# Performance work log

Hardware: AMD Instinct MI355X
Metric: run time of the kernel (lower is better)

Reference implementation:

```python
import jax, jax.numpy as jnp
import numpy as np


def setup_inputs() -> dict:
    key = jax.random.key(0)
    k1, k2 = jax.random.split(key)
    x = jax.random.normal(k1, (4, 4096, 128), dtype=jnp.float32)
    kernel = jax.random.normal(k2, (3, 128, 64), dtype=jnp.float32)
    return {"x": x, "kernel": kernel}


def reference(x, kernel):
    # QKV projections: x [B,N,Din] @ kernel[i] [Din,Dout] -> [B,N,Dout]
    WQ = jnp.einsum('bnd,de->bne', x, kernel[0])
    WK = jnp.einsum('bnd,de->bne', x, kernel[1])
    WV = jnp.einsum('bnd,de->bne', x, kernel[2])
    d_out = WV.shape[-1]
    # scaled dot-product scores [B,N,N]
    scores = jnp.einsum('bqe,bke->bqk', WQ, WK) / jnp.sqrt(jnp.float32(d_out))
    attn = jax.nn.softmax(scores, axis=-1)
    return jnp.einsum('bqk,bke->bqe', attn, WV)
```

## Files before the change

kernel.cpp:

```cpp
#include <hip/hip_runtime.h>


typedef __attribute__((ext_vector_type(8))) short bf16x8;
typedef __attribute__((ext_vector_type(16))) float f32x16;
typedef __attribute__((ext_vector_type(4))) unsigned u32x4;
typedef unsigned short us;

__device__ __forceinline__ us f2bf(float f) {
  unsigned u = __builtin_bit_cast(unsigned, f);
  u += 0x7FFFu + ((u >> 16) & 1u);
  return (us)(u >> 16);
}
__device__ __forceinline__ float bf2f(us h) {
  unsigned u = ((unsigned)h) << 16;
  return __builtin_bit_cast(float, u);
}
__device__ __forceinline__ f32x16 mfma(bf16x8 a, bf16x8 b, f32x16 c) {
  return __builtin_amdgcn_mfma_f32_32x32x16_bf16(a, b, c, 0, 0, 0);
}
__device__ __forceinline__ unsigned pk2t(float a, float b) {
  return __builtin_amdgcn_perm(__builtin_bit_cast(unsigned, b),
                               __builtin_bit_cast(unsigned, a), 0x07060302u);
}
__device__ __forceinline__ void dma16(const us* g, us* l) {
  __builtin_amdgcn_global_load_lds(
      (const __attribute__((address_space(1))) unsigned*)g,
      (__attribute__((address_space(3))) unsigned*)l, 16, 0, 0);
}
#define EXP2(x) __builtin_amdgcn_exp2f(x)

#define NSEG 16
#define ITERS 4

__global__ __launch_bounds__(256, 1) void wprep_kernel(
    const float* __restrict__ w, us* __restrict__ Wbh, us* __restrict__ Wbl)
{
  const int i = blockIdx.x * 256 + threadIdx.x;
  if (i >= 24576) return;
  const int p = i >> 13, d = (i & 8191) >> 6, e = i & 63;
  float v = w[i];
  if (p == 0) v *= 0.18033688011112042f;
  const us hi = f2bf(v);
  const us lo = f2bf(v - bf2f(hi));
  const int g = (p * 64 + e) >> 5, ks = d >> 4, hh = (d >> 3) & 1, j = d & 7;
  const int o = ((g * 8 + ks) * 2 + hh) * 256 + (e & 31) * 8 + j;
  Wbh[o] = hi;
  Wbl[o] = lo;
}

__global__ __launch_bounds__(384, 1) void qkv_kernel(
    const float* __restrict__ x,
    const us* __restrict__ Wbh, const us* __restrict__ Wbl,
    us* __restrict__ Qhi, us* __restrict__ Qlo,
    us* __restrict__ Kbh, us* __restrict__ Kbl, us* __restrict__ Vb)
{
  __shared__ unsigned ttile[32 * 193];
  const int t = threadIdx.x;
  const int rb = blockIdx.x;
  const int wid = t >> 6, lane = t & 63;
  const int l31 = lane & 31, h = lane >> 5;
  const int rbase = rb * 32;
  const float* xrow = x + (size_t)(rbase + l31) * 128;

  f32x16 acc = {};
  #pragma unroll
  for (int ks = 0; ks < 8; ++ks) {
    const int d0 = ks * 16 + h * 8;
    const float4 xa = *(const float4*)(xrow + d0);
    const float4 xb = *(const float4*)(xrow + d0 + 4);
    const float xv[8] = {xa.x, xa.y, xa.z, xa.w, xb.x, xb.y, xb.z, xb.w};
    bf16x8 ah, al;
    #pragma unroll
    for (int j = 0; j < 8; ++j) {
      us hi = f2bf(xv[j]);
      ah[j] = (short)hi;
      al[j] = (short)f2bf(xv[j] - bf2f(hi));
    }
    const int wo = ((wid * 8 + ks) * 2 + h) * 256 + l31 * 8;
    bf16x8 bh = *(const bf16x8*)(Wbh + wo);
    bf16x8 bl = *(const bf16x8*)(Wbl + wo);
    acc = mfma(ah, bh, acc);
    acc = mfma(al, bh, acc);
    acc = mfma(ah, bl, acc);
  }

  #pragma unroll
  for (int r = 0; r < 16; ++r) {
    const int rl = (r & 3) + 8 * (r >> 2) + 4 * h;
    float v = acc[r];
    us hi = f2bf(v);
    us lo = f2bf(v - bf2f(hi));
    ttile[rl * 193 + wid * 32 + l31] = (unsigned)hi | ((unsigned)lo << 16);
  }
  __syncthreads();

  if (t < 64) {
    const int row = t >> 1, cb = (t & 1) * 32;
    const int grow = rbase + row;
    unsigned hw[16], lw[16];
    #pragma unroll
    for (int j = 0; j < 16; ++j) {
      unsigned a = ttile[row * 193 + cb + 2 * j];
      unsigned bv = ttile[row * 193 + cb + 2 * j + 1];
      hw[j] = (a & 0xffffu) | (bv << 16);
      lw[j] = (a >> 16) | (bv & 0xffff0000u);
    }
    #pragma unroll
    for (int j = 0; j < 4; ++j) {
      uint4 hv = {hw[4 * j], hw[4 * j + 1], hw[4 * j + 2], hw[4 * j + 3]};
      uint4 lv = {lw[4 * j], lw[4 * j + 1], lw[4 * j + 2], lw[4 * j + 3]};
      *(uint4*)(Qhi + (size_t)grow * 64 + cb + 8 * j) = hv;
      *(uint4*)(Qlo + (size_t)grow * 64 + cb + 8 * j) = lv;
    }
  } else if (t < 192) {
    const int bb = rbase >> 12;
    const int kt = (rbase & 4095) >> 6;
    const int m = (rbase >> 5) & 1;
    const size_t kbb = (size_t)bb * 262144 + (size_t)kt * 4096 + m * 256;
    #pragma unroll
    for (int i2 = 0; i2 < 2; ++i2) {
      const int c = (t - 64) + 128 * i2;
      const int r = c & 31, hh = (c >> 5) & 1, ks = c >> 6;
      unsigned hw[4], lw[4];
      #pragma unroll
      for (int j = 0; j < 4; ++j) {
        unsigned a = ttile[r * 193 + 64 + 16 * ks + 8 * hh + 2 * j];
        unsigned bv = ttile[r * 193 + 64 + 16 * ks + 8 * hh + 2 * j + 1];
        hw[j] = (a & 0xffffu) | (bv << 16);
        lw[j] = (a >> 16) | (bv & 0xffff0000u);
      }
      const size_t off = kbb + (size_t)(ks * 4 + 2 * hh) * 256 + r * 8;
      uint4 hv = {hw[0], hw[1], hw[2], hw[3]};
      uint4 lv = {lw[0], lw[1], lw[2], lw[3]};
      *(uint4*)(Kbh + off) = hv;
      *(uint4*)(Kbl + off) = lv;
    }
  } else if (t < 320) {
    const int bb = rbase >> 12;
    const int nb = rbase & 4095;
    #pragma unroll
    for (int i2 = 0; i2 < 2; ++i2) {
      const int c = (t - 192) + 128 * i2;
      const int e = c >> 2, nc = c & 3;
      unsigned p[4];
      #pragma unroll
      for (int j = 0; j < 4; ++j) {
        unsigned a = ttile[(nc * 8 + 2 * j) * 193 + 128 + e];
        unsigned bv = ttile[(nc * 8 + 2 * j + 1) * 193 + 128 + e];
        p[j] = (a & 0xffffu) | (bv << 16);
      }
      uint4 pv = {p[0], p[1], p[2], p[3]};
      const int n0 = nb + nc * 8;
      const int kt = n0 >> 6, sub = n0 & 63;
      const int ks = sub >> 4, hh = (sub >> 3) & 1;
      const int dt = e >> 5, lv = e & 31;
      *(uint4*)(Vb + (size_t)bb * 262144 +
                ((((kt * 4 + ks) * 2 + hh) * 2 + dt) * 256 + lv * 8)) = pv;
    }
  }
}

__global__ __launch_bounds__(256, 3) void attn_kernel(
    const us* __restrict__ Qhi, const us* __restrict__ Qlo,
    const us* __restrict__ Kbh, const us* __restrict__ Kbl,
    const us* __restrict__ Vb,
    us* __restrict__ Opart, float* __restrict__ Mpart,
    float* __restrict__ Lpart)
{
  __shared__ us stage[2][12288];
  __shared__ float alds[4][32];

  const int bx = blockIdx.x;
  const int xc = bx & 7, b = xc >> 1;
  const int idx = ((bx >> 3) << 1) | (xc & 1);
  const int seg = idx & (NSEG - 1), qg = idx >> 4;
  const int t = threadIdx.x;
  const int wid = t >> 6, lane = t & 63;
  const int l31 = lane & 31, h = lane >> 5;
  const int q0 = qg * 128 + wid * 32;
  const int u = (b * 4096 + q0) >> 5;
  const size_t pb = (size_t)u * NSEG + seg;

  bf16x8 qh[4], ql[4];
  {
    const size_t rg = (size_t)(b * 4096 + q0 + l31) * 64;
    #pragma unroll
    for (int ks = 0; ks < 4; ++ks) {
      qh[ks] = *(const bf16x8*)(Qhi + rg + ks * 16 + h * 8);
      ql[ks] = *(const bf16x8*)(Qlo + rg + ks * 16 + h * 8);
    }
  }
  const size_t kbase = (size_t)b * 262144;

  {
    const size_t kb0 = kbase + (size_t)(seg * ITERS) * 4096;
    #pragma unroll
    for (int i = 0; i < 6; ++i) {
      const int c = wid * 6 + i;
      const us* src = (c < 8)  ? Kbh + kb0 + c * 512
                    : (c < 16) ? Kbl + kb0 + (c - 8) * 512
                               : Vb  + kb0 + (c - 16) * 512;
      dma16(src + lane * 8, &stage[0][c * 512]);
    }
  }
  __syncthreads();

  f32x16 o[2] = {};
  float mrun = -__builtin_inff();
  float lrun = 0.f;

  for (int it = 0; it < ITERS; ++it) {
    const int cur = it & 1;
    const us* sb = &stage[cur][0];

    if (it + 1 < ITERS) {
      const size_t kbn = kbase + (size_t)(seg * ITERS + it + 1) * 4096;
      #pragma unroll
      for (int i = 0; i < 6; ++i) {
        const int c = wid * 6 + i;
        const us* src = (c < 8)  ? Kbh + kbn + c * 512
                      : (c < 16) ? Kbl + kbn + (c - 8) * 512
                                 : Vb  + kbn + (c - 16) * 512;
        dma16(src + lane * 8, &stage[cur ^ 1][c * 512]);
      }
    }

    f32x16 s[2] = {};
    __builtin_amdgcn_s_setprio(1);
    #pragma unroll
    for (int ks = 0; ks < 4; ++ks) {
      #pragma unroll
      for (int m = 0; m < 2; ++m) {
        const int ko = (ks * 4 + 2 * h + m) * 256 + l31 * 8;
        const bf16x8 ah = *(const bf16x8*)(sb + ko);
        const bf16x8 al = *(const bf16x8*)(sb + 4096 + ko);
        s[m] = mfma(ah, qh[ks], s[m]);
        s[m] = mfma(al, qh[ks], s[m]);
        s[m] = mfma(ah, ql[ks], s[m]);
      }
    }
    __builtin_amdgcn_s_setprio(0);

    float va = fmaxf(s[0][0], s[1][0]);
    float vb = fmaxf(s[0][1], s[1][1]);
    #pragma unroll
    for (int r = 2; r < 16; r += 2) {
      va = fmaxf(va, fmaxf(s[0][r], s[1][r]));
      vb = fmaxf(vb, fmaxf(s[0][r + 1], s[1][r + 1]));
    }
    float vm = fmaxf(va, vb);
    vm = fmaxf(vm, __shfl_xor(vm, 32));

    if (!__all(vm <= mrun - 24.f)) {
      const float mnew = (vm > mrun + 0.5f) ? vm : mrun;
      const float alpha = EXP2(mrun - mnew);
      float sm0 = 0.f, sm1 = 0.f;
      unsigned pp[2][8];
      #pragma unroll
      for (int m = 0; m < 2; ++m) {
        #pragma unroll
        for (int p = 0; p < 8; ++p) {
          const float p0 = EXP2(s[m][2 * p] - mnew);
          const float p1 = EXP2(s[m][2 * p + 1] - mnew);
          sm0 += p0;
          sm1 += p1;
          pp[m][p] = pk2t(p0, p1);
        }
      }
      float sum = sm0 + sm1;
      sum += __shfl_xor(sum, 32);
      lrun = lrun * alpha + sum;
      mrun = mnew;

      if (__any(alpha != 1.f)) {
        if (!h) alds[wid][l31] = alpha;
        #pragma unroll
        for (int g = 0; g < 4; ++g) {
          const float4 af4 = *(const float4*)(&alds[wid][8 * g + 4 * h]);
          #pragma unroll
          for (int rr = 0; rr < 4; ++rr) {
            const int r = 4 * g + rr;
            const float a = (rr == 0) ? af4.x : (rr == 1) ? af4.y
                           : (rr == 2) ? af4.z : af4.w;
            o[0][r] *= a;
            o[1][r] *= a;
          }
        }
      }

      __builtin_amdgcn_s_setprio(1);
      #pragma unroll
      for (int ks = 0; ks < 4; ++ks) {
        const int vo = 8192 + (ks * 4 + 2 * h) * 256 + l31 * 8;
        const bf16x8 vf0 = *(const bf16x8*)(sb + vo);
        const bf16x8 vf1 = *(const bf16x8*)(sb + vo + 256);
        const int m = ks >> 1, base = 4 * (ks & 1);
        unsigned wx = pp[m][base + 0], wz = pp[m][base + 2];
        unsigned wy = pp[m][base + 1], ww = pp[m][base + 3];
        asm("v_permlane32_swap_b32 %0, %1" : "+v"(wx), "+v"(wz));
        asm("v_permlane32_swap_b32 %0, %1" : "+v"(wy), "+v"(ww));
        u32x4 wv;
        wv.x = wx;
        wv.y = wy;
        wv.z = wz;
        wv.w = ww;
        const bf16x8 af = __builtin_bit_cast(bf16x8, wv);
        o[0] = mfma(af, vf0, o[0]);
        o[1] = mfma(af, vf1, o[1]);
      }
      __builtin_amdgcn_s_setprio(0);
    }

    __syncthreads();
  }

  float* fw = ((float*)&stage[0][0]) + wid * (32 * 34);
  #pragma unroll
  for (int dt = 0; dt < 2; ++dt) {
    #pragma unroll
    for (int r = 0; r < 16; ++r) {
      const int qrow = (r & 3) + 8 * (r >> 2) + 4 * h;
      fw[qrow * 34 + l31] = o[dt][r];
    }
    #pragma unroll
    for (int jj = 0; jj < 2; ++jj) {
      const int chunk = lane + 64 * jj;
      const int rw = chunk >> 2, part = chunk & 3;
      const float* src = &fw[rw * 34 + part * 8];
      float2 a0 = *(const float2*)(src + 0);
      float2 a1 = *(const float2*)(src + 2);
      float2 a2 = *(const float2*)(src + 4);
      float2 a3 = *(const float2*)(src + 6);
      uint4 pkv;
      pkv.x = pk2t(a0.x, a0.y);
      pkv.y = pk2t(a1.x, a1.y);
      pkv.z = pk2t(a2.x, a2.y);
      pkv.w = pk2t(a3.x, a3.y);
      *(uint4*)(Opart + pb * 2048 + (size_t)rw * 64 + dt * 32 + part * 8) =
          pkv;
    }
  }
  if (!h) {
    Mpart[pb * 32 + l31] = mrun;
    Lpart[pb * 32 + l31] = lrun;
  }
}

__global__ __launch_bounds__(256, 1) void merge_kernel(
    const us* __restrict__ Opart, const float* __restrict__ Mpart,
    const float* __restrict__ Lpart, float* __restrict__ out)
{
  const int tg = blockIdx.x * 256 + threadIdx.x;
  const int q = tg >> 3, dc = (tg & 7) * 8;
  const int u = q >> 5, ql = q & 31;
  const int base = u * NSEG;
  float M = -__builtin_inff();
  #pragma unroll
  for (int s = 0; s < NSEG; ++s)
    M = fmaxf(M, Mpart[(size_t)(base + s) * 32 + ql]);
  float acc[8] = {};
  float den = 0.f;
  #pragma unroll
  for (int s = 0; s < NSEG; ++s) {
    const float wgt = EXP2(Mpart[(size_t)(base + s) * 32 + ql] - M);
    den += wgt * Lpart[(size_t)(base + s) * 32 + ql];
    const uint4 r = *(const uint4*)(Opart + (size_t)(base + s) * 2048 +
                                    ql * 64 + dc);
    const unsigned rw[4] = {r.x, r.y, r.z, r.w};
    #pragma unroll
    for (int j = 0; j < 4; ++j) {
      acc[2 * j]     += wgt * bf2f((us)(rw[j] & 0xffffu));
      acc[2 * j + 1] += wgt * bf2f((us)(rw[j] >> 16));
    }
  }
  const float inv = 1.f / den;
  float4 r0 = {acc[0] * inv, acc[1] * inv, acc[2] * inv, acc[3] * inv};
  float4 r1 = {acc[4] * inv, acc[5] * inv, acc[6] * inv, acc[7] * inv};
  *(float4*)(out + (size_t)q * 64 + dc) = r0;
  *(float4*)(out + (size_t)q * 64 + dc + 4) = r1;
}

extern "C" void kernel_launch(void* const* d_in, const int* in_sizes, int n_in,
                              void* d_out, int out_size, void* d_ws,
                              size_t ws_size, hipStream_t stream)
{
  const float* x = (const float*)d_in[0];
  const float* w = (const float*)d_in[1];
  float* out = (float*)d_out;
  char* ws = (char*)d_ws;

  const size_t T = 2097152;
  us* Qhi = (us*)(ws + 0 * T);
  us* Qlo = (us*)(ws + 1 * T);
  us* Kbh = (us*)(ws + 2 * T);
  us* Kbl = (us*)(ws + 3 * T);
  us* Vb  = (us*)(ws + 4 * T);
  us* Wbh = (us*)(ws + 5 * T);
  us* Wbl = (us*)(ws + 5 * T + 49152);
  char* pbase = ws + 5 * T + 98304;
  us* Opart = (us*)pbase;
  float* Mpart = (float*)(pbase + 33554432);
  float* Lpart = (float*)(pbase + 33554432 + 1048576);

  hipLaunchKernelGGL(wprep_kernel, dim3(96), dim3(256), 0, stream,
                     w, Wbh, Wbl);
  hipLaunchKernelGGL(qkv_kernel, dim3(512), dim3(384), 0, stream,
                     x, Wbh, Wbl, Qhi, Qlo, Kbh, Kbl, Vb);
  hipLaunchKernelGGL(attn_kernel, dim3(2048), dim3(256), 0, stream,
                     Qhi, Qlo, Kbh, Kbl, Vb, Opart, Mpart, Lpart);
  hipLaunchKernelGGL(merge_kernel, dim3(512), dim3(256), 0, stream,
                     Opart, Mpart, Lpart, out);
}
```

Measured before the change: 122.1 us.

## Fuse weight prep into QKV and split-KV merge into attention via counters

Drops the separate weight-prep kernel: each QKV wave now loads its fp32 weights directly and splits them into bf16 hi/lo in registers. Drops the separate merge kernel: each attention wave bumps an atomic counter per 32-query unit after writing its partials, and the last of the 16 segments merges them and writes the output. The counters are reset inside the QKV kernel. This saves two kernel launches and their gaps, but adds redundant weight loads and conversions in every QKV block and a serial merge tail on the last-arriving wave.

```diff
diff --git a/kernel.cpp b/kernel.cpp
--- a/kernel.cpp
+++ b/kernel.cpp
@@ -32,27 +32,11 @@
 #define NSEG 16
 #define ITERS 4
 
-__global__ __launch_bounds__(256, 1) void wprep_kernel(
-    const float* __restrict__ w, us* __restrict__ Wbh, us* __restrict__ Wbl)
-{
-  const int i = blockIdx.x * 256 + threadIdx.x;
-  if (i >= 24576) return;
-  const int p = i >> 13, d = (i & 8191) >> 6, e = i & 63;
-  float v = w[i];
-  if (p == 0) v *= 0.18033688011112042f;
-  const us hi = f2bf(v);
-  const us lo = f2bf(v - bf2f(hi));
-  const int g = (p * 64 + e) >> 5, ks = d >> 4, hh = (d >> 3) & 1, j = d & 7;
-  const int o = ((g * 8 + ks) * 2 + hh) * 256 + (e & 31) * 8 + j;
-  Wbh[o] = hi;
-  Wbl[o] = lo;
-}
-
 __global__ __launch_bounds__(384, 1) void qkv_kernel(
-    const float* __restrict__ x,
-    const us* __restrict__ Wbh, const us* __restrict__ Wbl,
+    const float* __restrict__ x, const float* __restrict__ w,
     us* __restrict__ Qhi, us* __restrict__ Qlo,
-    us* __restrict__ Kbh, us* __restrict__ Kbl, us* __restrict__ Vb)
+    us* __restrict__ Kbh, us* __restrict__ Kbl, us* __restrict__ Vb,
+    unsigned* __restrict__ cnt)
 {
   __shared__ unsigned ttile[32 * 193];
   const int t = threadIdx.x;
@@ -62,6 +46,24 @@
   const int rbase = rb * 32;
   const float* xrow = x + (size_t)(rbase + l31) * 128;
 
+  if (t == 0) cnt[rb] = 0;
+
+  bf16x8 wbh[8], wbl[8];
+  {
+    const float sc = (wid < 2) ? 0.18033688011112042f : 1.0f;
+    const float* wp = w + (wid >> 1) * 8192 + (wid & 1) * 32 + l31 + h * 512;
+    #pragma unroll
+    for (int ks = 0; ks < 8; ++ks) {
+      #pragma unroll
+      for (int j = 0; j < 8; ++j) {
+        const float v = wp[(ks * 16 + j) * 64] * sc;
+        const us hi = f2bf(v);
+        wbh[ks][j] = (short)hi;
+        wbl[ks][j] = (short)f2bf(v - bf2f(hi));
+      }
+    }
+  }
+
   f32x16 acc = {};
   #pragma unroll
   for (int ks = 0; ks < 8; ++ks) {
@@ -76,12 +78,9 @@
       ah[j] = (short)hi;
       al[j] = (short)f2bf(xv[j] - bf2f(hi));
     }
-    const int wo = ((wid * 8 + ks) * 2 + h) * 256 + l31 * 8;
-    bf16x8 bh = *(const bf16x8*)(Wbh + wo);
-    bf16x8 bl = *(const bf16x8*)(Wbl + wo);
-    acc = mfma(ah, bh, acc);
-    acc = mfma(al, bh, acc);
-    acc = mfma(ah, bl, acc);
+    acc = mfma(ah, wbh[ks], acc);
+    acc = mfma(al, wbh[ks], acc);
+    acc = mfma(ah, wbl[ks], acc);
   }
 
   #pragma unroll
@@ -165,7 +164,8 @@
     const us* __restrict__ Kbh, const us* __restrict__ Kbl,
     const us* __restrict__ Vb,
     us* __restrict__ Opart, float* __restrict__ Mpart,
-    float* __restrict__ Lpart)
+    float* __restrict__ Lpart, unsigned* __restrict__ cnt,
+    float* __restrict__ out)
 {
   __shared__ us stage[2][12288];
   __shared__ float alds[4][32];
@@ -344,40 +344,47 @@
     Mpart[pb * 32 + l31] = mrun;
     Lpart[pb * 32 + l31] = lrun;
   }
-}
-
-__global__ __launch_bounds__(256, 1) void merge_kernel(
-    const us* __restrict__ Opart, const float* __restrict__ Mpart,
-    const float* __restrict__ Lpart, float* __restrict__ out)
-{
-  const int tg = blockIdx.x * 256 + threadIdx.x;
-  const int q = tg >> 3, dc = (tg & 7) * 8;
-  const int u = q >> 5, ql = q & 31;
-  const int base = u * NSEG;
-  float M = -__builtin_inff();
-  #pragma unroll
-  for (int s = 0; s < NSEG; ++s)
-    M = fmaxf(M, Mpart[(size_t)(base + s) * 32 + ql]);
-  float acc[8] = {};
-  float den = 0.f;
-  #pragma unroll
-  for (int s = 0; s < NSEG; ++s) {
-    const float wgt = EXP2(Mpart[(size_t)(base + s) * 32 + ql] - M);
-    den += wgt * Lpart[(size_t)(base + s) * 32 + ql];
-    const uint4 r = *(const uint4*)(Opart + (size_t)(base + s) * 2048 +
-                                    ql * 64 + dc);
-    const unsigned rw[4] = {r.x, r.y, r.z, r.w};
-    #pragma unroll
-    for (int j = 0; j < 4; ++j) {
-      acc[2 * j]     += wgt * bf2f((us)(rw[j] & 0xffffu));
-      acc[2 * j + 1] += wgt * bf2f((us)(rw[j] >> 16));
-    }
-  }
-  const float inv = 1.f / den;
-  float4 r0 = {acc[0] * inv, acc[1] * inv, acc[2] * inv, acc[3] * inv};
-  float4 r1 = {acc[4] * inv, acc[5] * inv, acc[6] * inv, acc[7] * inv};
-  *(float4*)(out + (size_t)q * 64 + dc) = r0;
-  *(float4*)(out + (size_t)q * 64 + dc + 4) = r1;
+
+  __threadfence();
+  int old = 0;
+  if (lane == 0) old = (int)atomicAdd(&cnt[u], 1u);
+  old = __shfl(old, 0);
+  if (old == NSEG - 1) {
+    __threadfence();
+    const size_t ub = (size_t)u * NSEG;
+    const int q = l31, db = h;
+    float M = -__builtin_inff();
+    #pragma unroll
+    for (int s2 = 0; s2 < NSEG; ++s2)
+      M = fmaxf(M, Mpart[(ub + s2) * 32 + q]);
+    float den = 0.f;
+    float acc[32];
+    #pragma unroll
+    for (int k = 0; k < 32; ++k) acc[k] = 0.f;
+    for (int s2 = 0; s2 < NSEG; ++s2) {
+      const float wgt = EXP2(Mpart[(ub + s2) * 32 + q] - M);
+      den += wgt * Lpart[(ub + s2) * 32 + q];
+      const us* op = Opart + (ub + s2) * 2048 + q * 64 + db * 32;
+      #pragma unroll
+      for (int j = 0; j < 4; ++j) {
+        const uint4 r = *(const uint4*)(op + j * 8);
+        const unsigned rw4[4] = {r.x, r.y, r.z, r.w};
+        #pragma unroll
+        for (int j2 = 0; j2 < 4; ++j2) {
+          acc[j * 8 + 2 * j2]     += wgt * bf2f((us)(rw4[j2] & 0xffffu));
+          acc[j * 8 + 2 * j2 + 1] += wgt * bf2f((us)(rw4[j2] >> 16));
+        }
+      }
+    }
+    const float inv = 1.f / den;
+    float* op2 = out + ((size_t)u * 32 + q) * 64 + db * 32;
+    #pragma unroll
+    for (int j = 0; j < 8; ++j) {
+      float4 r0 = {acc[4 * j] * inv, acc[4 * j + 1] * inv,
+                   acc[4 * j + 2] * inv, acc[4 * j + 3] * inv};
+      *(float4*)(op2 + 4 * j) = r0;
+    }
+  }
 }
 
 extern "C" void kernel_launch(void* const* d_in, const int* in_sizes, int n_in,
@@ -395,19 +402,14 @@
   us* Kbh = (us*)(ws + 2 * T);
   us* Kbl = (us*)(ws + 3 * T);
   us* Vb  = (us*)(ws + 4 * T);
-  us* Wbh = (us*)(ws + 5 * T);
-  us* Wbl = (us*)(ws + 5 * T + 49152);
-  char* pbase = ws + 5 * T + 98304;
+  char* pbase = ws + 5 * T;
   us* Opart = (us*)pbase;
   float* Mpart = (float*)(pbase + 33554432);
   float* Lpart = (float*)(pbase + 33554432 + 1048576);
-
-  hipLaunchKernelGGL(wprep_kernel, dim3(96), dim3(256), 0, stream,
-                     w, Wbh, Wbl);
+  unsigned* cnt = (unsigned*)(pbase + 33554432 + 2097152);
+
   hipLaunchKernelGGL(qkv_kernel, dim3(512), dim3(384), 0, stream,
-                     x, Wbh, Wbl, Qhi, Qlo, Kbh, Kbl, Vb);
+                     x, w, Qhi, Qlo, Kbh, Kbl, Vb, cnt);
   hipLaunchKernelGGL(attn_kernel, dim3(2048), dim3(256), 0, stream,
-                     Qhi, Qlo, Kbh, Kbl, Vb, Opart, Mpart, Lpart);
-  hipLaunchKernelGGL(merge_kernel, dim3(512), dim3(256), 0, stream,
-                     Opart, Mpart, Lpart, out);
-}
+                     Qhi, Qlo, Kbh, Kbl, Vb, Opart, Mpart, Lpart, cnt, out);
+}
```

Result: slower. 414.9 us (+239.9%).
